# Kernel tuning notes

Measured on AMD Instinct MI355X. Metric: run time of the kernel, lower is better.

## Reference

```python
import jax, jax.numpy as jnp
import numpy as np

E, B, T = 7, 50, 100               # ensemble (network_size), no_batches=50, time blocks
D, A, L, H, C = 128, 32, 256, 1024, 128  # data, action, latent, hidden, context sizes
H_STEP = 0.1                        # (t1 - t0) / T == dt -> one SDE step per block


def setup_inputs() -> dict:
    key = jax.random.key(0)
    ks = iter(jax.random.split(key, 64))
    def nrm(shape, scale=1.0):
        return jax.random.normal(next(ks), shape, jnp.float32) * scale
    def ens(i, o):
        s = 1.0 / np.sqrt(i)
        return nrm((E, i, o), s), nrm((E, o), s)
    def lin(i, o):
        s = 1.0 / np.sqrt(i)
        return nrm((i, o), s), nrm((o,), s)
    inp = {}
    inp["enc_w1"], inp["enc_b1"] = ens(D, H)
    inp["enc_w2"], inp["enc_b2"] = ens(H, H)
    inp["enc_w3"], inp["enc_b3"] = ens(H, C)
    inp["qz0_w"], inp["qz0_b"] = ens(C, 2 * L)
    inp["act_w"], inp["act_b"] = ens(L + A + D, L)
    inp["proj_w1"], inp["proj_b1"] = ens(L, H)
    inp["proj_w2"], inp["proj_b2"] = ens(H, H)
    inp["proj_w3"], inp["proj_b3"] = ens(H, D)
    inp["f_w1"], inp["f_b1"] = lin(L, H)
    inp["f_w2"], inp["f_b2"] = lin(H, H)
    inp["f_w3"], inp["f_b3"] = lin(H, L)
    inp["h_w1"], inp["h_b1"] = lin(L, H)
    inp["h_w2"], inp["h_b2"] = lin(H, H)
    inp["h_w3"], inp["h_b3"] = lin(H, L)
    # per-latent-dim g nets: Linear(1,H) -> ReLU -> Linear(H,1), stacked over L dims
    inp["g_w1"] = nrm((L, H), 0.2)
    inp["g_b1"] = nrm((L, H), 0.2)
    inp["g_w2"] = nrm((L, H), 0.2 / np.sqrt(H))
    inp["g_b2"] = 0.5 + nrm((L,), 0.01)   # keep diffusion bounded away from 0
    inp["pz0_mean"] = jnp.zeros((E, 1, L), jnp.float32)
    inp["pz0_logstd"] = jnp.zeros((E, 1, L), jnp.float32)
    inp["xs"] = nrm((E, T * B, D))
    inp["actions"] = nrm((E, T * B, A))
    inp["eps_z0"] = nrm((T, E, B, L))      # torch.randn_like noise for z0 reparam
    inp["dw_noise"] = nrm((T, E * B, L))   # Brownian increment noise (unit std)
    return inp


def reference(enc_w1, enc_b1, enc_w2, enc_b2, enc_w3, enc_b3,
              qz0_w, qz0_b, act_w, act_b,
              proj_w1, proj_b1, proj_w2, proj_b2, proj_w3, proj_b3,
              f_w1, f_b1, f_w2, f_b2, f_w3, f_b3,
              h_w1, h_b1, h_w2, h_b2, h_w3, h_b3,
              g_w1, g_b1, g_w2, g_b2,
              pz0_mean, pz0_logstd,
              xs, actions, eps_z0, dw_noise):
    def ens_lin(x, w, b):  # EnsembleFC: bmm + bias
        return jnp.einsum('ebi,eio->ebo', x, w) + b[:, None, :]

    def encoder(x):
        x = jax.nn.relu(ens_lin(x, enc_w1, enc_b1))
        x = jax.nn.relu(ens_lin(x, enc_w2, enc_b2))
        return ens_lin(x, enc_w3, enc_b3)

    def projector(z):
        z = jnp.tanh(ens_lin(z, proj_w1, proj_b1))
        z = jnp.tanh(ens_lin(z, proj_w2, proj_b2))
        return ens_lin(z, proj_w3, proj_b3)

    def mlp(y, w1, b1, w2, b2, w3, b3):  # Linear-ReLU-Linear-Tanh-Linear
        y = jax.nn.relu(y @ w1 + b1)
        y = jnp.tanh(y @ w2 + b2)
        return y @ w3 + b3

    def g_fn(y):  # vectorized per-dim tiny MLPs: y (N, L) -> (N, L)
        hh = jax.nn.relu(y[:, :, None] * g_w1[None] + g_b1[None])  # (N, L, H)
        return jnp.sum(hh * g_w2[None], axis=-1) + g_b2

    xs_t = jnp.moveaxis(xs.reshape(E, T, B, D), 1, 0)        # (T, E, B, D)
    act_t = jnp.moveaxis(actions.reshape(E, T, B, A), 1, 0)  # (T, E, B, A)
    sqrt_h = jnp.sqrt(jnp.float32(H_STEP))

    def step(carry, inps):
        zs_last, i = carry
        x_i, a_i, eps_i, dw_i = inps
        ctx = encoder(x_i)                                  # (E, B, C)
        q = ens_lin(ctx, qz0_w, qz0_b)                      # (E, B, 2L)
        qm, ql = q[..., :L], q[..., L:]
        z0 = qm + jnp.exp(ql) * eps_i
        z_in = jnp.where(i == 0, z0, zs_last)               # first step uses z0
        lad = jnp.concatenate([z_in, a_i, x_i], axis=2)
        z = ens_lin(lad, act_w, act_b).reshape(E * B, L)
        # one SDE step with logqp (f: posterior drift, h: prior drift, g: diffusion)
        fv = mlp(z, f_w1, f_b1, f_w2, f_b2, f_w3, f_b3)
        hv = mlp(z, h_w1, h_b1, h_w2, h_b2, h_w3, h_b3)
        gv = g_fn(z)
        u = (fv - hv) / gv
        lr = 0.5 * jnp.sum(u * u, axis=-1) * H_STEP         # (E*B,) log-ratio increment
        z_new = z + fv * H_STEP + gv * (sqrt_h * dw_i)
        zs_new = z_new.reshape(E, B, L)
        xm = projector(zs_new)                              # (E, B, D)
        # KL(q(z0) || p(z0)) for diagonal Gaussians
        kl = (pz0_logstd - ql) \
             + (jnp.exp(2.0 * ql) + (qm - pz0_mean) ** 2) / (2.0 * jnp.exp(2.0 * pz0_logstd)) \
             - 0.5
        logqp0 = kl.sum(axis=2).mean(axis=1)                # (E,)
        lr_mean = lr.reshape(E, B).mean(axis=1)             # (E,)
        return (zs_new, i + 1), (lr_mean, logqp0, xm)

    init = (jnp.zeros((E, B, L), xs.dtype), jnp.int32(0))
    (_, _), (lrm, lq0, xms) = jax.lax.scan(step, init, (xs_t, act_t, eps_z0, dw_noise))
    logqp_path = lrm.sum(axis=0) + lq0.sum(axis=0)          # (E,)
    predicted_xs = jnp.moveaxis(xms, 0, 1).reshape(E, T * B, D)
    return logqp_path, predicted_xs
```

## Files before the change

kernel.cpp:

```cpp
#include <hip/hip_runtime.h>
#include <hip/hip_bf16.h>
#include <math.h>

#define E_ 7
#define B_ 50
#define T_ 100
#define D_ 128
#define A_ 32
#define L_ 256
#define H_ 1024
#define C_ 128
#define EB_ 350
#define TB_ 5000
#define SQRTH 0.31622776601683794f

typedef __attribute__((ext_vector_type(8))) short s8v;
typedef __attribute__((ext_vector_type(4))) float f32x4;
typedef _Float16 f16x2 __attribute__((ext_vector_type(2)));
typedef __hip_bfloat16 bf16;

#define MFMA __builtin_amdgcn_mfma_f32_16x16x32_bf16

__device__ __forceinline__ int lswz(int row, int ck) {
  return ((ck & ~7) | ((ck ^ row) & 7)) << 3;
}

struct BG {
  const bf16* A[8];
  const bf16* W[8];
  const float* bias[8];
  float* Cf[8];
  bf16* Cb[8];
};

template<int BM, int ACT, int OUT>
__global__ __launch_bounds__(256)
void bgemm(BG g, int M, int K, int lda, int ldw, int ldc) {
  __shared__ short As[BM * 64];
  __shared__ short Ws[128 * 64];
  const short* Ap = (const short*)g.A[blockIdx.z];
  const short* Wp = (const short*)g.W[blockIdx.z];
  const int bm = blockIdx.x * BM, bn = blockIdx.y * 128;
  const int tid = threadIdx.x;
  const int wv = tid >> 6, lane = tid & 63;
  const int wm0 = (wv >> 1) * (BM / 2), wn0 = (wv & 1) * 64;
  const int l15 = lane & 15, l4 = lane >> 4;
  constexpr int FM = BM / 32;
  constexpr int AI = BM / 32;
  f32x4 acc[FM][4] = {};
  for (int k0 = 0; k0 < K; k0 += 64) {
    s8v av[AI], wvv[4];
#pragma unroll
    for (int i = 0; i < AI; ++i) {
      const int c = tid + i * 256, r = c >> 3, ck = c & 7;
      s8v v = {};
      if (bm + r < M) v = *(const s8v*)(Ap + (size_t)(bm + r) * lda + k0 + ck * 8);
      av[i] = v;
// ... 108 lines not shown
  const bf16 h = __float2bfloat16(w);
  const size_t fo = (size_t)e * 65536 + ((size_t)(n >> 4) * 8 + (k >> 5)) * 512 +
                    (((k >> 3) & 3) << 7) + ((n & 15) << 3) + (k & 7);
  hi[fo] = h;
  lo[fo] = __float2bfloat16(w - __bfloat162float(h));
}

__global__ __launch_bounds__(256)
void ax_build(const float* __restrict__ actions, const float* __restrict__ xs,
              bf16* __restrict__ dst) {
  const int idx = blockIdx.x * 256 + threadIdx.x;
  if (idx >= E_ * TB_ * 192) return;
  const int k = idx % 192;
  const int r = (idx / 192) % TB_;
  const int e = idx / (192 * TB_);
  float v = 0.f;
  if (k < 32) v = actions[((size_t)e * TB_ + r) * A_ + k];
  else if (k < 160) v = xs[((size_t)e * TB_ + r) * D_ + (k - 32)];
  dst[idx] = __float2bfloat16(v);
}

__global__ __launch_bounds__(256)
void waxT_build(const float* __restrict__ act_w, bf16* __restrict__ dst) {
  const int idx = blockIdx.x * 256 + threadIdx.x;
  if (idx >= E_ * 256 * 192) return;
  const int k = idx % 192;
  const int n = (idx / 192) % 256;
  const int e = idx / (192 * 256);
  float v = (k < 160) ? act_w[(size_t)e * 416 * 256 + (size_t)(256 + k) * 256 + n] : 0.f;
  dst[idx] = __float2bfloat16(v);
}

__global__ __launch_bounds__(256)
void gpack_build(const float* __restrict__ gw1, const float* __restrict__ gb1,
                 const float* __restrict__ gw2, _Float16* __restrict__ dst) {
  const int idx = blockIdx.x * 256 + threadIdx.x;
  if (idx >= 256 * 3 * 1024) return;
  const int l = idx / 3072, rem = idx - l * 3072, arr = rem >> 10, h = rem & 1023;
  const float* s = arr == 0 ? gw1 : (arr == 1 ? gb1 : gw2);
  dst[idx] = (_Float16)s[(size_t)l * 1024 + h];
}

__global__ __launch_bounds__(256)
void qkl_kernel(const float* __restrict__ ctx, int rows, int row_off, int ctx_estride,
                const float* __restrict__ qw, const float* __restrict__ qb,
                const float* __restrict__ pm, const float* __restrict__ pl,
                const float* __restrict__ eps0, bf16* __restrict__ z0hi,
                bf16* __restrict__ z0lo, float* __restrict__ logqp) {
  __shared__ float cx[16][128];
  __shared__ float red[16];
  const int e = blockIdx.y;
  const int r0 = blockIdx.x * 16;
  const int tid = threadIdx.x;
  {
    const int r = tid >> 4, c = (tid & 15) * 8;
    float4 v0 = make_float4(0.f, 0.f, 0.f, 0.f), v1 = v0;
    if (r0 + r < rows) {
      const float* src = ctx + (size_t)e * ctx_estride + (size_t)(r0 + r) * C_ + c;
      v0 = *(const float4*)src;
      v1 = *(const float4*)(src + 4);
    }
    *(float4*)&cx[r][c] = v0;
    *(float4*)&cx[r][c + 4] = v1;
  }
  if (tid < 16) red[tid] = 0.f;
  __syncthreads();
  const int j = tid;
  const float* w = qw + (size_t)e * C_ * 512;
  float am_[16] = {};
  float al_[16] = {};
  for (int k0 = 0; k0 < C_; k0 += 4) {
    float wm[4], wl[4];
#pragma unroll
// ... 11 lines not shown
        al_[r] = fmaf(cc[q], wl[q], al_[r]);
      }
    }
  }
  const float qbm = qb[(size_t)e * 512 + j];
  const float qbl = qb[(size_t)e * 512 + 256 + j];
  const float pmv = pm[(size_t)e * L_ + j];
  const float plv = pl[(size_t)e * L_ + j];
  const float inv2e = 0.5f * expf(-2.f * plv);
#pragma unroll
  for (int r = 0; r < 16; ++r) {
    float kl = 0.f;
    if (r0 + r < rows) {
      const float qm_ = am_[r] + qbm;
      const float ql_ = al_[r] + qbl;
      const float dm = qm_ - pmv;
      kl = plv - ql_ + (expf(2.f * ql_) + dm * dm) * inv2e - 0.5f;
      const int gi = row_off + r0 + r;
      if (gi < B_) {
        const size_t zi = ((size_t)e * B_ + gi) * L_ + j;
        const float z0 = qm_ + expf(ql_) * eps0[zi];
        const bf16 h = __float2bfloat16(z0);
        z0hi[zi] = h;
        z0lo[zi] = __float2bfloat16(z0 - __bfloat162float(h));
      }
    }
    for (int off = 32; off; off >>= 1) kl += __shfl_xor(kl, off, 64);
    if ((tid & 63) == 0) atomicAdd(&red[r], kl);
  }
  __syncthreads();
  if (tid < 16 && r0 + tid < rows) atomicAdd(&logqp[e], red[tid] * (1.0f / B_));
}

__global__ __launch_bounds__(256, 2)
void k1_act(const bf16* __restrict__ zhi, const bf16* __restrict__ zlo,
            const bf16* __restrict__ wzh, const bf16* __restrict__ wzl,
            const float* __restrict__ axw, float* __restrict__ zP,
            bf16* __restrict__ zPb, int t) {
  __shared__ short Ah[16 * 256];
  __shared__ short Al[16 * 256];
  const int e = blockIdx.z, rb = blockIdx.x, nb = blockIdx.y * 128;
  const int r0 = rb * 13;
  const int nrows = (50 - r0 < 13) ? (50 - r0) : 13;
  const int tid = threadIdx.x, lane = tid & 63, wv = tid >> 6;
  const int l15 = lane & 15, l4 = lane >> 4;
  const short* zh = (const short*)zhi + (size_t)(e * 50 + r0) * 256;
  const short* zl = (const short*)zlo + (size_t)(e * 50 + r0) * 256;
#pragma unroll
  for (int i = 0; i < 2; ++i) {
    const int lin = tid + i * 256, row = lin >> 5, ck = lin & 31;
    s8v vh = {}, vl = {};
    if (row < nrows) {
      vh = *(const s8v*)(zh + row * 256 + ck * 8);
      vl = *(const s8v*)(zl + row * 256 + ck * 8);
    }
    *(s8v*)(Ah + row * 256 + lswz(row, ck)) = vh;
    *(s8v*)(Al + row * 256 + lswz(row, ck)) = vl;
  }
  __syncthreads();
  const short* Bh = (const short*)wzh + (size_t)e * 65536;
  const short* Bl = (const short*)wzl + (size_t)e * 65536;
  f32x4 acc[2] = {};
#pragma unroll
  for (int kt = 0; kt < 8; ++kt) {
    const int ck = kt * 4 + l4;
    const s8v ah = *(const s8v*)(Ah + l15 * 256 + lswz(l15, ck));
    const s8v al = *(const s8v*)(Al + l15 * 256 + lswz(l15, ck));
#pragma unroll
    for (int nt = 0; nt < 2; ++nt) {
      const int ng = nb + wv * 32 + nt * 16;
      const size_t bo = ((size_t)(ng >> 4) * 8 + kt) * 512 + lane * 8;
      const s8v bh = *(const s8v*)(Bh + bo);
      const s8v bl = *(const s8v*)(Bl + bo);
      acc[nt] = MFMA(ah, bh, acc[nt], 0, 0, 0);
      acc[nt] = MFMA(al, bh, acc[nt], 0, 0, 0);
      acc[nt] = MFMA(ah, bl, acc[nt], 0, 0, 0);
    }
  }
#pragma unroll
  for (int nt = 0; nt < 2; ++nt) {
    const int col = nb + wv * 32 + nt * 16 + l15;
#pragma unroll
    for (int j = 0; j < 4; ++j) {
      const int row = l4 * 4 + j;
      if (row < nrows) {
        const int gr = e * 50 + r0 + row;
        const float v = acc[nt][j] + axw[((size_t)e * TB_ + t * 50 + r0 + row) * 256 + col];
        zP[(size_t)gr * 256 + col] = v;
        zPb[(size_t)gr * 256 + col] = __float2bfloat16(v);
      }
    }
  }
}

__global__ __launch_bounds__(256, 2)
void k2_l1(const bf16* __restrict__ zPb, const bf16* __restrict__ w1f,
           const float* __restrict__ fb1, const float* __restrict__ hb1,
           bf16* __restrict__ fh1) {
  __shared__ short As[16 * 256];
  const int rb = blockIdx.x, nb = blockIdx.y * 128;
  const int r0 = rb * 16;
  const int tid = threadIdx.x, lane = tid & 63, wv = tid >> 6;
  const int l15 = lane & 15, l4 = lane >> 4;
#pragma unroll
  for (int i = 0; i < 2; ++i) {
    const int lin = tid + i * 256, row = lin >> 5, ck = lin & 31;
    s8v v = {};
    if (r0 + row < EB_)
      v = *(const s8v*)((const short*)zPb + (size_t)(r0 + row) * 256 + ck * 8);
    *(s8v*)(As + row * 256 + lswz(row, ck)) = v;
  }
  __syncthreads();
  f32x4 acc[2] = {};
#pragma unroll
  for (int kt = 0; kt < 8; ++kt) {
    const int ck = kt * 4 + l4;
    const s8v a = *(const s8v*)(As + l15 * 256 + lswz(l15, ck));
#pragma unroll
    for (int nt = 0; nt < 2; ++nt) {
      const int ng = nb + wv * 32 + nt * 16;
      const s8v b = *(const s8v*)((const short*)w1f + ((size_t)(ng >> 4) * 8 + kt) * 512 + lane * 8);
      acc[nt] = MFMA(a, b, acc[nt], 0, 0, 0);
    }
  }
#pragma unroll
  for (int nt = 0; nt < 2; ++nt) {
    const int col = nb + wv * 32 + nt * 16 + l15;
    const float bv = (col < 1024) ? fb1[col] : hb1[col - 1024];
#pragma unroll
    for (int j = 0; j < 4; ++j) {
      const int row = r0 + l4 * 4 + j;
      if (row < EB_)
        fh1[(size_t)row * 2048 + col] = __float2bfloat16(fmaxf(acc[nt][j] + bv, 0.f));
    }
  }
}

__global__ __launch_bounds__(256, 2)
void k3_l2(const bf16* __restrict__ fh1, const bf16* __restrict__ w2f,
           const float* __restrict__ fb2, const float* __restrict__ hb2,
           bf16* __restrict__ fh2) {
  __shared__ short As[16 * 1024];
  const int rb = blockIdx.x, nbl = blockIdx.y;
  const int nb = nbl * 128, r0 = rb * 16;
  const int half = (nbl >= 8) ? 1024 : 0;
  const int tid = threadIdx.x, lane = tid & 63, wv = tid >> 6;
  const int l15 = lane & 15, l4 = lane >> 4;
#pragma unroll
  for (int i = 0; i < 8; ++i) {
    const int lin = tid + i * 256, row = lin >> 7, ck = lin & 127;
    s8v v = {};
    if (r0 + row < EB_)
      v = *(const s8v*)((const short*)fh1 + (size_t)(r0 + row) * 2048 + half + ck * 8);
    *(s8v*)(As + row * 1024 + lswz(row, ck)) = v;
  }
  __syncthreads();
  f32x4 acc[2] = {};
#pragma unroll 4
  for (int kt = 0; kt < 32; ++kt) {
    const int ck = kt * 4 + l4;
    const s8v a = *(const s8v*)(As + l15 * 1024 + lswz(l15, ck));
#pragma unroll
    for (int nt = 0; nt < 2; ++nt) {
      const int ng = nb + wv * 32 + nt * 16;
      const s8v b = *(const s8v*)((const short*)w2f + ((size_t)(ng >> 4) * 32 + kt) * 512 + lane * 8);
      acc[nt] = MFMA(a, b, acc[nt], 0, 0, 0);
    }
  }
#pragma unroll
  for (int nt = 0; nt < 2; ++nt) {
    const int col = nb + wv * 32 + nt * 16 + l15;
    const float bv = half ? hb2[col - 1024] : fb2[col];
#pragma unroll
    for (int j = 0; j < 4; ++j) {
      const int row = r0 + l4 * 4 + j;
      if (row < EB_)
        fh2[(size_t)row * 2048 + col] = __float2bfloat16(tanhf(acc[nt][j] + bv));
    }
  }
}

__global__ __launch_bounds__(256, 1)
void k4_fin(const bf16* __restrict__ fh2, const bf16* __restrict__ w3f,
            const float* __restrict__ fb3, const float* __restrict__ hb3,
            const _Float16* __restrict__ gpk, const float* __restrict__ gb2,
            const float* __restrict__ zP, const float* __restrict__ dw,
            bf16* __restrict__ zhi, bf16* __restrict__ zlo,
            bf16* __restrict__ zs_bf, float* __restrict__ logqp, int t) {
  __shared__ short As[16 * 1024];
  __shared__ float ztile[16][64];
  __shared__ float gvt[16][64];
  __shared__ float ebuck[8];
  const int rb = blockIdx.x, cb = blockIdx.y;
  const int r0 = rb * 16, c0 = cb * 64;
  const int tid = threadIdx.x, lane = tid & 63, wv = tid >> 6;
  const int l15 = lane & 15, l4 = lane >> 4;
  if (tid < 8) ebuck[tid] = 0.f;
#pragma unroll
  for (int i = 0; i < 4; ++i) {
    const int lin = tid + i * 256, row = lin >> 6, col = lin & 63;
    ztile[row][col] = (r0 + row < EB_) ? zP[(size_t)(r0 + row) * 256 + c0 + col] : 1.0f;
  }
  f32x4 accF = {}, accH = {};
#pragma unroll
  for (int fb = 0; fb < 2; ++fb) {
    __syncthreads();
#pragma unroll
    for (int i = 0; i < 8; ++i) {
      const int lin = tid + i * 256, row = lin >> 7, ck = lin & 127;
      s8v v = {};
      if (r0 + row < EB_)
        v = *(const s8v*)((const short*)fh2 + (size_t)(r0 + row) * 2048 + fb * 1024 + ck * 8);
      *(s8v*)(As + row * 1024 + lswz(row, ck)) = v;
    }
    __syncthreads();
    const int ng = fb * 256 + c0 + wv * 16;
    f32x4 acc = {};
#pragma unroll 4
    for (int kt = 0; kt < 32; ++kt) {
      const int ck = kt * 4 + l4;
      const s8v a = *(const s8v*)(As + l15 * 1024 + lswz(l15, ck));
      const s8v b = *(const s8v*)((const short*)w3f + ((size_t)(ng >> 4) * 32 + kt) * 512 + lane * 8);
      acc = MFMA(a, b, acc, 0, 0, 0);
    }
    if (fb) accH = acc; else accF = acc;
  }
  __syncthreads();
  {
    const int lloc = tid >> 2, hq = tid & 3;
    const _Float16* gl = gpk + (size_t)(c0 + lloc) * 3072 + hq * 256;
    f16x2 z2[16];
#pragma unroll
    for (int r = 0; r < 16; ++r) {
      const _Float16 zh_ = (_Float16)ztile[r][lloc];
      z2[r] = f16x2{zh_, zh_};
    }
    float ga[16] = {};
    for (int hp = 0; hp < 128; ++hp) {
      const f16x2 w1v = *(const f16x2*)(gl + 2 * hp);
      const f16x2 b1v = *(const f16x2*)(gl + 1024 + 2 * hp);
      const f16x2 w2v = *(const f16x2*)(gl + 2048 + 2 * hp);
#pragma unroll
      for (int r = 0; r < 16; ++r) {
        f16x2 tt = z2[r] * w1v + b1v;
#if __has_builtin(__builtin_elementwise_max)
        const f16x2 zz = {};
        tt = __builtin_elementwise_max(tt, zz);
#else
        tt[0] = tt[0] > (_Float16)0 ? tt[0] : (_Float16)0;
        tt[1] = tt[1] > (_Float16)0 ? tt[1] : (_Float16)0;
#endif
#if __has_builtin(__builtin_amdgcn_fdot2)
        ga[r] = __builtin_amdgcn_fdot2(tt, w2v, ga[r], false);
#else
        ga[r] += (float)tt[0] * (float)w2v[0] + (float)tt[1] * (float)w2v[1];
#endif
      }
    }
#pragma unroll
    for (int r = 0; r < 16; ++r) {
      float v = ga[r];
      v += __shfl_xor(v, 1, 64);
      v += __shfl_xor(v, 2, 64);
      if (hq == 0) gvt[r][lloc] = v + gb2[c0 + lloc];
    }
  }
  __syncthreads();
  const int col_loc = wv * 16 + l15, col = c0 + col_loc;
  const float fb3v = fb3[col], hb3v = hb3[col];
#pragma unroll
  for (int j = 0; j < 4; ++j) {
    const int rl = l4 * 4 + j, row = r0 + rl;
    if (row < EB_) {
      const float fv = accF[j] + fb3v;
      const float hv = accH[j] + hb3v;
      const float gv = gvt[rl][col_loc];
      const float u = (fv - hv) / gv;
      atomicAdd(&ebuck[row / 50], 0.001f * u * u);
      const float znew = ztile[rl][col_loc] + 0.1f * fv +
                         gv * (SQRTH * dw[(size_t)t * (EB_ * 256) + (size_t)row * 256 + col]);
      const bf16 h = __float2bfloat16(znew);
      const size_t zi = (size_t)row * 256 + col;
      zhi[zi] = h;
      zlo[zi] = __float2bfloat16(znew - __bfloat162float(h));
      const int e = row / 50, b = row - e * 50;
      zs_bf[((size_t)e * TB_ + t * 50 + b) * 256 + col] = h;
    }
  }
  __syncthreads();
  if (tid < 7) {
    const float v = ebuck[tid];
    if (v != 0.f) atomicAdd(&logqp[tid], v);
  }
}

__global__ void init_kernel(float* logqp) {
  if (threadIdx.x < E_) logqp[threadIdx.x] = 0.f;
}

extern "C" void kernel_launch(void* const* d_in, const int* in_sizes, int n_in,
                              void* d_out, int out_size, void* d_ws, size_t ws_size,
                              hipStream_t stream) {
  (void)in_sizes; (void)n_in; (void)out_size;
  const float* enc_w1 = (const float*)d_in[0];
  const float* enc_b1 = (const float*)d_in[1];
  const float* enc_w2 = (const float*)d_in[2];
  const float* enc_b2 = (const float*)d_in[3];
  const float* enc_w3 = (const float*)d_in[4];
  const float* enc_b3 = (const float*)d_in[5];
  const float* qz0_w  = (const float*)d_in[6];
  const float* qz0_b  = (const float*)d_in[7];
  const float* act_w  = (const float*)d_in[8];
  const float* act_b  = (const float*)d_in[9];
  const float* proj_w1 = (const float*)d_in[10];
  const float* proj_b1 = (const float*)d_in[11];
  const float* proj_w2 = (const float*)d_in[12];
  const float* proj_b2 = (const float*)d_in[13];
  const float* proj_w3 = (const float*)d_in[14];
  const float* proj_b3 = (const float*)d_in[15];
  const float* f_w1 = (const float*)d_in[16];
  const float* f_b1 = (const float*)d_in[17];
  const float* f_w2 = (const float*)d_in[18];
  const float* f_b2 = (const float*)d_in[19];
  const float* f_w3 = (const float*)d_in[20];
  const float* f_b3 = (const float*)d_in[21];
  const float* h_w1 = (const float*)d_in[22];
  const float* h_b1 = (const float*)d_in[23];
  const float* h_w2 = (const float*)d_in[24];
  const float* h_b2 = (const float*)d_in[25];
  const float* h_w3 = (const float*)d_in[26];
  const float* h_b3 = (const float*)d_in[27];
  const float* g_w1 = (const float*)d_in[28];
  const float* g_b1 = (const float*)d_in[29];
  const float* g_w2 = (const float*)d_in[30];
  const float* g_b2 = (const float*)d_in[31];
  const float* pz0_mean   = (const float*)d_in[32];
  const float* pz0_logstd = (const float*)d_in[33];
  const float* xs      = (const float*)d_in[34];
  const float* actions = (const float*)d_in[35];
  const float* eps_z0  = (const float*)d_in[36];
  const float* dw      = (const float*)d_in[37];

  float* out = (float*)d_out;
  float* logqp = out;
  float* pred = out + E_;

  char* base = (char*)d_ws;
  size_t off = 0;
  auto alloc = [&](size_t bytes) {
    void* p = base + off;
    off = (off + bytes + 255) & ~(size_t)255;
    return p;
  };
  bf16* zhi    = (bf16*)alloc((size_t)EB_ * 256 * 2);
  bf16* zlo    = (bf16*)alloc((size_t)EB_ * 256 * 2);
  float* zP    = (float*)alloc((size_t)EB_ * 256 * 4);
  bf16* zPb    = (bf16*)alloc((size_t)EB_ * 256 * 2);
  bf16* fh1    = (bf16*)alloc((size_t)EB_ * 2048 * 2);
  bf16* fh2    = (bf16*)alloc((size_t)EB_ * 2048 * 2);
  bf16* zs_bf  = (bf16*)alloc((size_t)E_ * T_ * B_ * 256 * 2);
  float* axw   = (float*)alloc((size_t)E_ * TB_ * 256 * 4);
  bf16* ax_bf  = (bf16*)alloc((size_t)E_ * TB_ * 192 * 2);
  bf16* waxT   = (bf16*)alloc((size_t)E_ * 256 * 192 * 2);
  bf16* wzh    = (bf16*)alloc((size_t)E_ * 65536 * 2);
  bf16* wzl    = (bf16*)alloc((size_t)E_ * 65536 * 2);
  bf16* w1f    = (bf16*)alloc((size_t)2048 * 256 * 2);
  bf16* w2f    = (bf16*)alloc((size_t)2048 * 1024 * 2);
  bf16* w3f    = (bf16*)alloc((size_t)512 * 1024 * 2);
  _Float16* gpk = (_Float16*)alloc((size_t)256 * 3 * 1024 * 2);
  bf16* xs_bf  = (bf16*)alloc((size_t)E_ * TB_ * D_ * 2);
  bf16* ew1T = (bf16*)alloc((size_t)E_ * D_ * H_ * 2);
  bf16* ew2T = (bf16*)alloc((size_t)E_ * H_ * H_ * 2);
  bf16* ew3T = (bf16*)alloc((size_t)E_ * H_ * C_ * 2);
  bf16* pw1T = (bf16*)alloc((size_t)E_ * L_ * H_ * 2);
  bf16* pw2T = (bf16*)alloc((size_t)E_ * H_ * H_ * 2);
  bf16* pw3T = (bf16*)alloc((size_t)E_ * H_ * D_ * 2);
  const size_t per_row = (size_t)E_ * (H_ * 2 * 2 + C_ * 4);
  size_t remain = (ws_size > off + 4096) ? (ws_size - off - 4096) : 0;
  int CH = (int)(remain / per_row);
  if (CH > 2500) CH = 2500;
  if (CH < 64) CH = 64;
  bf16* bufA = (bf16*)alloc((size_t)E_ * CH * H_ * 2);
  bf16* bufB = (bf16*)alloc((size_t)E_ * CH * H_ * 2);
  float* bufC = (float*)alloc((size_t)E_ * CH * C_ * 4);

  init_kernel<<<dim3(1), dim3(64), 0, stream>>>(logqp);

  const dim3 cb256(256);
  cvt_kernel<<<dim3((E_ * TB_ * D_ / 4 + 255) / 256), cb256, 0, stream>>>(xs, xs_bf, E_ * TB_ * D_ / 4);
  cvtT_kernel<<<dim3(H_ / 32, D_ / 32, E_), cb256, 0, stream>>>(enc_w1, ew1T, D_, H_, (long)D_ * H_, (long)D_ * H_);
  cvtT_kernel<<<dim3(H_ / 32, H_ / 32, E_), cb256, 0, stream>>>(enc_w2, ew2T, H_, H_, (long)H_ * H_, (long)H_ * H_);
  cvtT_kernel<<<dim3(C_ / 32, H_ / 32, E_), cb256, 0, stream>>>(enc_w3, ew3T, H_, C_, (long)H_ * C_, (long)H_ * C_);
  cvtT_kernel<<<dim3(H_ / 32, L_ / 32, E_), cb256, 0, stream>>>(proj_w1, pw1T, L_, H_, (long)L_ * H_, (long)L_ * H_);
  cvtT_kernel<<<dim3(H_ / 32, H_ / 32, E_), cb256, 0, stream>>>(proj_w2, pw2T, H_, H_, (long)H_ * H_, (long)H_ * H_);
  cvtT_kernel<<<dim3(D_ / 32, H_ / 32, E_), cb256, 0, stream>>>(proj_w3, pw3T, H_, D_, (long)H_ * D_, (long)H_ * D_);
  ax_build<<<dim3((E_ * TB_ * 192 + 255) / 256), cb256, 0, stream>>>(actions, xs, ax_bf);
  waxT_build<<<dim3((E_ * 256 * 192 + 255) / 256), cb256, 0, stream>>>(act_w, waxT);
  packWz<<<dim3((E_ * 65536 + 255) / 256), cb256, 0, stream>>>(act_w, wzh, wzl);
  packW<<<dim3((256 * 1024 + 255) / 256), cb256, 0, stream>>>(f_w1, w1f, 256, 1024);
  packW<<<dim3((256 * 1024 + 255) / 256), cb256, 0, stream>>>(h_w1, w1f + (size_t)1024 * 256, 256, 1024);
  packW<<<dim3((1024 * 1024 + 255) / 256), cb256, 0, stream>>>(f_w2, w2f, 1024, 1024);
  packW<<<dim3((1024 * 1024 + 255) / 256), cb256, 0, stream>>>(h_w2, w2f + (size_t)1024 * 1024, 1024, 1024);
  packW<<<dim3((1024 * 256 + 255) / 256), cb256, 0, stream>>>(f_w3, w3f, 1024, 256);
  packW<<<dim3((1024 * 256 + 255) / 256), cb256, 0, stream>>>(h_w3, w3f + (size_t)256 * 1024, 1024, 256);
  gpack_build<<<dim3((256 * 3 * 1024 + 255) / 256), cb256, 0, stream>>>(g_w1, g_b1, g_w2, gpk);

  BG g;
  for (int e = 0; e < E_; ++e) {
    g.A[e] = ax_bf + (size_t)e * TB_ * 192;
    g.W[e] = waxT + (size_t)e * 256 * 192;
    g.bias[e] = act_b + (size_t)e * 256;
    g.Cf[e] = axw + (size_t)e * TB_ * 256;
  }
  bgemm<128, 0, 0><<<dim3((TB_ + 127) / 128, 2, E_), 256, 0, stream>>>(g, TB_, 192, 192, 192, 256);

  for (int c = 0; c < TB_; c += CH) {
    const int rows = (TB_ - c < CH) ? (TB_ - c) : CH;
    const int mt = (rows + 127) / 128;
    for (int e = 0; e < E_; ++e) {
      g.A[e] = xs_bf + ((size_t)e * TB_ + c) * D_;
      g.W[e] = ew1T + (size_t)e * D_ * H_;
      g.bias[e] = enc_b1 + (size_t)e * H_;
      g.Cb[e] = bufA + (size_t)e * CH * H_;
    }
    bgemm<128, 1, 1><<<dim3(mt, H_ / 128, E_), 256, 0, stream>>>(g, rows, D_, D_, D_, H_);
    for (int e = 0; e < E_; ++e) {
      g.A[e] = bufA + (size_t)e * CH * H_;
      g.W[e] = ew2T + (size_t)e * H_ * H_;
      g.bias[e] = enc_b2 + (size_t)e * H_;
      g.Cb[e] = bufB + (size_t)e * CH * H_;
    }
    bgemm<128, 1, 1><<<dim3(mt, H_ / 128, E_), 256, 0, stream>>>(g, rows, H_, H_, H_, H_);
    for (int e = 0; e < E_; ++e) {
      g.A[e] = bufB + (size_t)e * CH * H_;
      g.W[e] = ew3T + (size_t)e * H_ * C_;
      g.bias[e] = enc_b3 + (size_t)e * C_;
      g.Cf[e] = bufC + (size_t)e * CH * C_;
    }
    bgemm<128, 0, 0><<<dim3(mt, C_ / 128, E_), 256, 0, stream>>>(g, rows, H_, H_, H_, C_);
    qkl_kernel<<<dim3((rows + 15) / 16, E_), 256, 0, stream>>>(
        bufC, rows, c, CH * C_, qz0_w, qz0_b, pz0_mean, pz0_logstd, eps_z0,
        zhi, zlo, logqp);
  }

  for (int t = 0; t < T_; ++t) {
    k1_act<<<dim3(4, 2, E_), 256, 0, stream>>>(zhi, zlo, wzh, wzl, axw, zP, zPb, t);
    k2_l1<<<dim3(22, 16), 256, 0, stream>>>(zPb, w1f, f_b1, h_b1, fh1);
    k3_l2<<<dim3(22, 16), 256, 0, stream>>>(fh1, w2f, f_b2, h_b2, fh2);
    k4_fin<<<dim3(22, 4), 256, 0, stream>>>(fh2, w3f, f_b3, h_b3, gpk, g_b2,
                                            zP, dw, zhi, zlo, zs_bf, logqp, t);
  }

  for (int c = 0; c < TB_; c += CH) {
    const int rows = (TB_ - c < CH) ? (TB_ - c) : CH;
    const int mt = (rows + 127) / 128;
    for (int e = 0; e < E_; ++e) {
      g.A[e] = zs_bf + ((size_t)e * T_ * B_ + c) * L_;
      g.W[e] = pw1T + (size_t)e * L_ * H_;
      g.bias[e] = proj_b1 + (size_t)e * H_;
      g.Cb[e] = bufA + (size_t)e * CH * H_;
    }
    bgemm<128, 2, 1><<<dim3(mt, H_ / 128, E_), 256, 0, stream>>>(g, rows, L_, L_, L_, H_);
    for (int e = 0; e < E_; ++e) {
      g.A[e] = bufA + (size_t)e * CH * H_;
      g.W[e] = pw2T + (size_t)e * H_ * H_;
      g.bias[e] = proj_b2 + (size_t)e * H_;
      g.Cb[e] = bufB + (size_t)e * CH * H_;
    }
    bgemm<128, 2, 1><<<dim3(mt, H_ / 128, E_), 256, 0, stream>>>(g, rows, H_, H_, H_, H_);
    for (int e = 0; e < E_; ++e) {
      g.A[e] = bufB + (size_t)e * CH * H_;
      g.W[e] = pw3T + (size_t)e * H_ * D_;
      g.bias[e] = proj_b3 + (size_t)e * D_;
      g.Cf[e] = pred + ((size_t)e * TB_ + c) * D_;
    }
    bgemm<128, 0, 0><<<dim3(mt, D_ / 128, E_), 256, 0, stream>>>(g, rows, H_, H_, H_, D_);
  }
}
```

Baseline: 10.30 ms.

## Fuse action-latent GEMM with first f/h MLP layer into one kernel

Merges k1_act and k2_l1 into a single kernel per ensemble member and column tile. Each block recomputes the full 50x256 action-latent projection into shared memory as bf16, then runs the first f/h layer from it, which removes one launch per time step and the zPb round trip through global memory. In exchange the projection GEMM is computed redundantly in all 16 column blocks, and the launch uses fewer, larger blocks (112) with 96KB of shared memory each, which lowers occupancy.

```diff
diff --git a/kernel.cpp b/kernel.cpp
--- a/kernel.cpp
+++ b/kernel.cpp
@@ -22,7 +22,11 @@
 #define MFMA __builtin_amdgcn_mfma_f32_16x16x32_bf16
 
 __device__ __forceinline__ int lswz(int row, int ck) {
-  return ((ck & ~7) | ((ck ^ row) & 7)) << 3;
+  return (((ck & ~7) | ((ck ^ row) & 7)) << 3);
+}
+__device__ __forceinline__ int swzE(int r, int col) {
+  const int ck = col >> 3;
+  return (((ck & ~7) | ((ck ^ r) & 7)) << 3) + (col & 7);
 }
 
 struct BG {
@@ -281,106 +285,87 @@
   if (tid < 16 && r0 + tid < rows) atomicAdd(&logqp[e], red[tid] * (1.0f / B_));
 }
 
-__global__ __launch_bounds__(256, 2)
-void k1_act(const bf16* __restrict__ zhi, const bf16* __restrict__ zlo,
+__global__ __launch_bounds__(256)
+void akt_l1(const bf16* __restrict__ zhi, const bf16* __restrict__ zlo,
             const bf16* __restrict__ wzh, const bf16* __restrict__ wzl,
-            const float* __restrict__ axw, float* __restrict__ zP,
-            bf16* __restrict__ zPb, int t) {
-  __shared__ short Ah[16 * 256];
-  __shared__ short Al[16 * 256];
-  const int e = blockIdx.z, rb = blockIdx.x, nb = blockIdx.y * 128;
-  const int r0 = rb * 13;
-  const int nrows = (50 - r0 < 13) ? (50 - r0) : 13;
+            const float* __restrict__ axw, const bf16* __restrict__ w1f,
+            const float* __restrict__ fb1, const float* __restrict__ hb1,
+            float* __restrict__ zP, bf16* __restrict__ fh1, int t) {
+  __shared__ short Zh[64 * 256];
+  __shared__ short Zl[64 * 256];
+  __shared__ short Pb[64 * 256];
+  const int e = blockIdx.y, nt1 = blockIdx.x;
   const int tid = threadIdx.x, lane = tid & 63, wv = tid >> 6;
   const int l15 = lane & 15, l4 = lane >> 4;
-  const short* zh = (const short*)zhi + (size_t)(e * 50 + r0) * 256;
-  const short* zl = (const short*)zlo + (size_t)(e * 50 + r0) * 256;
-#pragma unroll
-  for (int i = 0; i < 2; ++i) {
-    const int lin = tid + i * 256, row = lin >> 5, ck = lin & 31;
+  for (int i = tid; i < 64 * 32; i += 256) {
+    const int row = i >> 5, ck = i & 31;
     s8v vh = {}, vl = {};
-    if (row < nrows) {
-      vh = *(const s8v*)(zh + row * 256 + ck * 8);
-      vl = *(const s8v*)(zl + row * 256 + ck * 8);
-    }
-    *(s8v*)(Ah + row * 256 + lswz(row, ck)) = vh;
-    *(s8v*)(Al + row * 256 + lswz(row, ck)) = vl;
+    if (row < 50) {
+      vh = *(const s8v*)((const short*)zhi + (size_t)(e * 50 + row) * 256 + ck * 8);
+      vl = *(const s8v*)((const short*)zlo + (size_t)(e * 50 + row) * 256 + ck * 8);
+    }
+    *(s8v*)(Zh + row * 256 + lswz(row, ck)) = vh;
+    *(s8v*)(Zl + row * 256 + lswz(row, ck)) = vl;
   }
   __syncthreads();
   const short* Bh = (const short*)wzh + (size_t)e * 65536;
   const short* Bl = (const short*)wzl + (size_t)e * 65536;
-  f32x4 acc[2] = {};
-#pragma unroll
-  for (int kt = 0; kt < 8; ++kt) {
-    const int ck = kt * 4 + l4;
-    const s8v ah = *(const s8v*)(Ah + l15 * 256 + lswz(l15, ck));
-    const s8v al = *(const s8v*)(Al + l15 * 256 + lswz(l15, ck));
-#pragma unroll
-    for (int nt = 0; nt < 2; ++nt) {
-      const int ng = nb + wv * 32 + nt * 16;
-      const size_t bo = ((size_t)(ng >> 4) * 8 + kt) * 512 + lane * 8;
-      const s8v bh = *(const s8v*)(Bh + bo);
-      const s8v bl = *(const s8v*)(Bl + bo);
-      acc[nt] = MFMA(ah, bh, acc[nt], 0, 0, 0);
-      acc[nt] = MFMA(al, bh, acc[nt], 0, 0, 0);
-      acc[nt] = MFMA(ah, bl, acc[nt], 0, 0, 0);
-    }
-  }
-#pragma unroll
-  for (int nt = 0; nt < 2; ++nt) {
-    const int col = nb + wv * 32 + nt * 16 + l15;
-#pragma unroll
-    for (int j = 0; j < 4; ++j) {
-      const int row = l4 * 4 + j;
-      if (row < nrows) {
-        const int gr = e * 50 + r0 + row;
-        const float v = acc[nt][j] + axw[((size_t)e * TB_ + t * 50 + r0 + row) * 256 + col];
-        zP[(size_t)gr * 256 + col] = v;
-        zPb[(size_t)gr * 256 + col] = __float2bfloat16(v);
-      }
-    }
-  }
-}
-
-__global__ __launch_bounds__(256, 2)
-void k2_l1(const bf16* __restrict__ zPb, const bf16* __restrict__ w1f,
-           const float* __restrict__ fb1, const float* __restrict__ hb1,
-           bf16* __restrict__ fh1) {
-  __shared__ short As[16 * 256];
-  const int rb = blockIdx.x, nb = blockIdx.y * 128;
-  const int r0 = rb * 16;
-  const int tid = threadIdx.x, lane = tid & 63, wv = tid >> 6;
-  const int l15 = lane & 15, l4 = lane >> 4;
-#pragma unroll
-  for (int i = 0; i < 2; ++i) {
-    const int lin = tid + i * 256, row = lin >> 5, ck = lin & 31;
-    s8v v = {};
-    if (r0 + row < EB_)
-      v = *(const s8v*)((const short*)zPb + (size_t)(r0 + row) * 256 + ck * 8);
-    *(s8v*)(As + row * 256 + lswz(row, ck)) = v;
-  }
-  __syncthreads();
-  f32x4 acc[2] = {};
-#pragma unroll
-  for (int kt = 0; kt < 8; ++kt) {
-    const int ck = kt * 4 + l4;
-    const s8v a = *(const s8v*)(As + l15 * 256 + lswz(l15, ck));
-#pragma unroll
-    for (int nt = 0; nt < 2; ++nt) {
-      const int ng = nb + wv * 32 + nt * 16;
-      const s8v b = *(const s8v*)((const short*)w1f + ((size_t)(ng >> 4) * 8 + kt) * 512 + lane * 8);
-      acc[nt] = MFMA(a, b, acc[nt], 0, 0, 0);
-    }
-  }
-#pragma unroll
-  for (int nt = 0; nt < 2; ++nt) {
-    const int col = nb + wv * 32 + nt * 16 + l15;
-    const float bv = (col < 1024) ? fb1[col] : hb1[col - 1024];
-#pragma unroll
-    for (int j = 0; j < 4; ++j) {
-      const int row = r0 + l4 * 4 + j;
-      if (row < EB_)
-        fh1[(size_t)row * 2048 + col] = __float2bfloat16(fmaxf(acc[nt][j] + bv, 0.f));
+#pragma unroll
+  for (int c2 = 0; c2 < 4; ++c2) {
+    const int ct = wv * 4 + c2;
+#pragma unroll
+    for (int rt = 0; rt < 4; ++rt) {
+      f32x4 acc = {};
+#pragma unroll
+      for (int kt = 0; kt < 8; ++kt) {
+        const int ck = kt * 4 + l4;
+        const int ar = rt * 16 + l15;
+        const s8v ah = *(const s8v*)(Zh + ar * 256 + lswz(ar, ck));
+        const s8v al = *(const s8v*)(Zl + ar * 256 + lswz(ar, ck));
+        const size_t bo = ((size_t)(ct * 8 + kt)) * 512 + (size_t)lane * 8;
+        const s8v bh = *(const s8v*)(Bh + bo);
+        const s8v bl = *(const s8v*)(Bl + bo);
+        acc = MFMA(ah, bh, acc, 0, 0, 0);
+        acc = MFMA(al, bh, acc, 0, 0, 0);
+        acc = MFMA(ah, bl, acc, 0, 0, 0);
+      }
+      const int col = ct * 16 + l15;
+#pragma unroll
+      for (int j = 0; j < 4; ++j) {
+        const int r = rt * 16 + l4 * 4 + j;
+        float v = 0.f;
+        if (r < 50)
+          v = acc[j] + axw[((size_t)(e * TB_) + t * 50 + r) * 256 + col];
+        *(bf16*)&Pb[r * 256 + swzE(r, col)] = __float2bfloat16(v);
+        if (nt1 == 0 && r < 50) zP[(size_t)(e * 50 + r) * 256 + col] = v;
+      }
+    }
+  }
+  __syncthreads();
+#pragma unroll
+  for (int c2 = 0; c2 < 2; ++c2) {
+    const int gct = nt1 * 8 + wv * 2 + c2;
+#pragma unroll
+    for (int rt = 0; rt < 4; ++rt) {
+      f32x4 acc = {};
+#pragma unroll
+      for (int kt = 0; kt < 8; ++kt) {
+        const int ck = kt * 4 + l4;
+        const int ar = rt * 16 + l15;
+        const s8v av = *(const s8v*)(Pb + ar * 256 + lswz(ar, ck));
+        const s8v bv = *(const s8v*)((const short*)w1f +
+                                     ((size_t)(gct * 8 + kt)) * 512 + (size_t)lane * 8);
+        acc = MFMA(av, bv, acc, 0, 0, 0);
+      }
+      const int col = gct * 16 + l15;
+      const float bv_ = (col < 1024) ? fb1[col] : hb1[col - 1024];
+#pragma unroll
+      for (int j = 0; j < 4; ++j) {
+        const int r = rt * 16 + l4 * 4 + j;
+        if (r < 50)
+          fh1[(size_t)(e * 50 + r) * 2048 + col] =
+              __float2bfloat16(fmaxf(acc[j] + bv_, 0.f));
+      }
     }
   }
 }
@@ -604,7 +589,6 @@
   bf16* zhi    = (bf16*)alloc((size_t)EB_ * 256 * 2);
   bf16* zlo    = (bf16*)alloc((size_t)EB_ * 256 * 2);
   float* zP    = (float*)alloc((size_t)EB_ * 256 * 4);
-  bf16* zPb    = (bf16*)alloc((size_t)EB_ * 256 * 2);
   bf16* fh1    = (bf16*)alloc((size_t)EB_ * 2048 * 2);
   bf16* fh2    = (bf16*)alloc((size_t)EB_ * 2048 * 2);
   bf16* zs_bf  = (bf16*)alloc((size_t)E_ * T_ * B_ * 256 * 2);
@@ -693,8 +677,8 @@
   }
 
   for (int t = 0; t < T_; ++t) {
-    k1_act<<<dim3(4, 2, E_), 256, 0, stream>>>(zhi, zlo, wzh, wzl, axw, zP, zPb, t);
-    k2_l1<<<dim3(22, 16), 256, 0, stream>>>(zPb, w1f, f_b1, h_b1, fh1);
+    akt_l1<<<dim3(16, E_), 256, 0, stream>>>(zhi, zlo, wzh, wzl, axw, w1f,
+                                             f_b1, h_b1, zP, fh1, t);
     k3_l2<<<dim3(22, 16), 256, 0, stream>>>(fh1, w2f, f_b2, h_b2, fh2);
     k4_fin<<<dim3(22, 4), 256, 0, stream>>>(fh2, w3f, f_b3, h_b3, gpk, g_b2,
                                             zP, dw, zhi, zlo, zs_bf, logqp, t);
```

New measurement: 11.53 ms. 1.12x slower.

## Fuse SDE finalize with next step's action and layer-1 GEMMs per ensemble

Applied to the files above, without the earlier changes.

Replaces the per-step k4_fin/k1_act/k2_l1 sequence with one kernel, kfin, plus k3_l2, so each time step launches two kernels instead of four. Each kfin block owns a quarter of one ensemble's batch rows across all 256 latent columns. It computes the layer-3 drift outputs, the g diffusion net, the state update, the next action projection, and the next layer-1 activations while keeping z in shared memory. The g-weight packing is reordered for coalesced half2 loads, and the log-ratio sum is reduced per block. In exchange the fused kernel runs only 28 blocks of 512 threads, which lowers parallelism and could make each step slower despite fewer launches and less global traffic.

```diff
diff --git a/kernel.cpp b/kernel.cpp
--- a/kernel.cpp
+++ b/kernel.cpp
@@ -22,7 +22,28 @@
 #define MFMA __builtin_amdgcn_mfma_f32_16x16x32_bf16
 
 __device__ __forceinline__ int lswz(int row, int ck) {
-  return ((ck & ~7) | ((ck ^ row) & 7)) << 3;
+  return (((ck & ~7) | ((ck ^ row) & 7)) << 3);
+}
+__device__ __forceinline__ int swzE(int r, int col) {
+  const int ck = col >> 3;
+  return (((ck & ~7) | ((ck ^ r) & 7)) << 3) + (col & 7);
+}
+__device__ __forceinline__ f16x2 relu2(f16x2 t) {
+#if __has_builtin(__builtin_elementwise_max)
+  const f16x2 zz = {};
+  return __builtin_elementwise_max(t, zz);
+#else
+  t[0] = t[0] > (_Float16)0 ? t[0] : (_Float16)0;
+  t[1] = t[1] > (_Float16)0 ? t[1] : (_Float16)0;
+  return t;
+#endif
+}
+__device__ __forceinline__ float fdot2a(f16x2 a, f16x2 b, float c) {
+#if __has_builtin(__builtin_amdgcn_fdot2)
+  return __builtin_amdgcn_fdot2(a, b, c, false);
+#else
+  return c + (float)a[0] * (float)b[0] + (float)a[1] * (float)b[1];
+#endif
 }
 
 struct BG {
@@ -197,13 +218,16 @@
 }
 
 __global__ __launch_bounds__(256)
-void gpack_build(const float* __restrict__ gw1, const float* __restrict__ gb1,
-                 const float* __restrict__ gw2, _Float16* __restrict__ dst) {
+void gpack2(const float* __restrict__ gw1, const float* __restrict__ gb1,
+            const float* __restrict__ gw2, _Float16* __restrict__ dst) {
   const int idx = blockIdx.x * 256 + threadIdx.x;
-  if (idx >= 256 * 3 * 1024) return;
-  const int l = idx / 3072, rem = idx - l * 3072, arr = rem >> 10, h = rem & 1023;
+  if (idx >= 3 * 512 * 256 * 2) return;
+  const int i = idx & 1;
+  const int l = (idx >> 1) & 255;
+  const int hpg = (idx >> 9) & 511;
+  const int arr = idx >> 18;
   const float* s = arr == 0 ? gw1 : (arr == 1 ? gb1 : gw2);
-  dst[idx] = (_Float16)s[(size_t)l * 1024 + h];
+  dst[idx] = (_Float16)s[(size_t)l * 1024 + hpg * 2 + i];
 }
 
 __global__ __launch_bounds__(256)
@@ -429,117 +453,197 @@
   }
 }
 
-__global__ __launch_bounds__(256, 1)
-void k4_fin(const bf16* __restrict__ fh2, const bf16* __restrict__ w3f,
-            const float* __restrict__ fb3, const float* __restrict__ hb3,
-            const _Float16* __restrict__ gpk, const float* __restrict__ gb2,
-            const float* __restrict__ zP, const float* __restrict__ dw,
-            bf16* __restrict__ zhi, bf16* __restrict__ zlo,
-            bf16* __restrict__ zs_bf, float* __restrict__ logqp, int t) {
+__global__ __launch_bounds__(512)
+void kfin(const bf16* __restrict__ fh2, const bf16* __restrict__ w3f,
+          const float* __restrict__ fb3, const float* __restrict__ hb3,
+          const _Float16* __restrict__ gpk, const float* __restrict__ gb2,
+          float* __restrict__ zP, const float* __restrict__ dw,
+          const float* __restrict__ axw, const bf16* __restrict__ wzh,
+          const bf16* __restrict__ wzl, const bf16* __restrict__ w1f,
+          const float* __restrict__ fb1, const float* __restrict__ hb1,
+          bf16* __restrict__ zs_bf, bf16* __restrict__ fh1,
+          float* __restrict__ logqp, int t, int doAct) {
   __shared__ short As[16 * 1024];
-  __shared__ float ztile[16][64];
-  __shared__ float gvt[16][64];
-  __shared__ float ebuck[8];
-  const int rb = blockIdx.x, cb = blockIdx.y;
-  const int r0 = rb * 16, c0 = cb * 64;
-  const int tid = threadIdx.x, lane = tid & 63, wv = tid >> 6;
+  __shared__ float zst[16 * 256];
+  __shared__ float gvt[16 * 256];
+  __shared__ short Zh[16 * 256];
+  __shared__ short Zl[16 * 256];
+  __shared__ short Pb[16 * 256];
+  __shared__ float red[8];
+  const int bx = blockIdx.x;
+  const int e = bx >> 2, q = bx & 3;
+  const int nr = (q < 2) ? 13 : 12;
+  const int b0 = (q < 2) ? q * 13 : 26 + (q - 2) * 12;
+  const int R0 = e * 50 + b0;
+  const int tid = threadIdx.x, wave = tid >> 6, lane = tid & 63;
   const int l15 = lane & 15, l4 = lane >> 4;
-  if (tid < 8) ebuck[tid] = 0.f;
-#pragma unroll
-  for (int i = 0; i < 4; ++i) {
-    const int lin = tid + i * 256, row = lin >> 6, col = lin & 63;
-    ztile[row][col] = (r0 + row < EB_) ? zP[(size_t)(r0 + row) * 256 + c0 + col] : 1.0f;
-  }
-  f32x4 accF = {}, accH = {};
-#pragma unroll
-  for (int fb = 0; fb < 2; ++fb) {
+  for (int i = tid; i < 4096; i += 512) {
+    const int r = i >> 8, c = i & 255;
+    zst[i] = (r < nr) ? zP[(size_t)(R0 + r) * 256 + c] : 0.f;
+  }
+  for (int i = tid; i < 2048; i += 512) {
+    const int row = i >> 7, ck = i & 127;
+    s8v v = {};
+    if (row < nr) v = *(const s8v*)((const short*)fh2 + (size_t)(R0 + row) * 2048 + ck * 8);
+    *(s8v*)(As + row * 1024 + lswz(row, ck)) = v;
+  }
+  __syncthreads();
+  f32x4 accF[2] = {}, accH[2] = {};
+#pragma unroll 4
+  for (int kt = 0; kt < 32; ++kt) {
+    const int ck = kt * 4 + l4;
+    const s8v a = *(const s8v*)(As + l15 * 1024 + lswz(l15, ck));
+#pragma unroll
+    for (int cc = 0; cc < 2; ++cc) {
+      const int ct = wave * 2 + cc;
+      const s8v b = *(const s8v*)((const short*)w3f + ((size_t)(ct * 32 + kt)) * 512 + (size_t)lane * 8);
+      accF[cc] = MFMA(a, b, accF[cc], 0, 0, 0);
+    }
+  }
+  __syncthreads();
+  for (int i = tid; i < 2048; i += 512) {
+    const int row = i >> 7, ck = i & 127;
+    s8v v = {};
+    if (row < nr) v = *(const s8v*)((const short*)fh2 + (size_t)(R0 + row) * 2048 + 1024 + ck * 8);
+    *(s8v*)(As + row * 1024 + lswz(row, ck)) = v;
+  }
+  __syncthreads();
+#pragma unroll 4
+  for (int kt = 0; kt < 32; ++kt) {
+    const int ck = kt * 4 + l4;
+    const s8v a = *(const s8v*)(As + l15 * 1024 + lswz(l15, ck));
+#pragma unroll
+    for (int cc = 0; cc < 2; ++cc) {
+      const int ct = 16 + wave * 2 + cc;
+      const s8v b = *(const s8v*)((const short*)w3f + ((size_t)(ct * 32 + kt)) * 512 + (size_t)lane * 8);
+      accH[cc] = MFMA(a, b, accH[cc], 0, 0, 0);
+    }
+  }
+  {
+    const int hh = wave >> 2;
+    const int l = tid & 255;
+    f16x2 z2[13];
+    float ga[13];
+#pragma unroll
+    for (int r = 0; r < 13; ++r) {
+      const _Float16 z = (_Float16)zst[r * 256 + l];
+      z2[r] = f16x2{z, z};
+      ga[r] = 0.f;
+    }
+    const _Float16* gb_ = gpk + (size_t)(hh * 256) * 512 + (size_t)l * 2;
+    for (int k = 0; k < 256; ++k) {
+      const size_t o = (size_t)k * 512;
+      const f16x2 w1 = *(const f16x2*)(gb_ + o);
+      const f16x2 b1 = *(const f16x2*)(gb_ + 262144 + o);
+      const f16x2 w2 = *(const f16x2*)(gb_ + 524288 + o);
+#pragma unroll
+      for (int r = 0; r < 13; ++r)
+        ga[r] = fdot2a(relu2(z2[r] * w1 + b1), w2, ga[r]);
+    }
+    if (hh == 0) {
+#pragma unroll
+      for (int r = 0; r < 13; ++r) gvt[r * 256 + l] = ga[r];
+    }
     __syncthreads();
-#pragma unroll
-    for (int i = 0; i < 8; ++i) {
-      const int lin = tid + i * 256, row = lin >> 7, ck = lin & 127;
-      s8v v = {};
-      if (r0 + row < EB_)
-        v = *(const s8v*)((const short*)fh2 + (size_t)(r0 + row) * 2048 + fb * 1024 + ck * 8);
-      *(s8v*)(As + row * 1024 + lswz(row, ck)) = v;
-    }
-    __syncthreads();
-    const int ng = fb * 256 + c0 + wv * 16;
+    if (hh == 1) {
+#pragma unroll
+      for (int r = 0; r < 13; ++r) gvt[r * 256 + l] += ga[r] + gb2[l];
+    }
+  }
+  __syncthreads();
+  float lr = 0.f;
+#pragma unroll
+  for (int cc = 0; cc < 2; ++cc) {
+    const int col = (wave * 2 + cc) * 16 + l15;
+    const float fb3v = fb3[col], hb3v = hb3[col];
+#pragma unroll
+    for (int j = 0; j < 4; ++j) {
+      const int r = l4 * 4 + j;
+      if (r < nr) {
+        const float fv = accF[cc][j] + fb3v;
+        const float hv = accH[cc][j] + hb3v;
+        const float gv = gvt[r * 256 + col];
+        const float u = (fv - hv) / gv;
+        lr += u * u;
+        const float zn = zst[r * 256 + col] + 0.1f * fv +
+            gv * (SQRTH * dw[(size_t)t * (EB_ * 256) + (size_t)(R0 + r) * 256 + col]);
+        zst[r * 256 + col] = zn;
+        zs_bf[((size_t)e * TB_ + t * 50 + b0 + r) * 256 + col] = __float2bfloat16(zn);
+      }
+    }
+  }
+#pragma unroll
+  for (int o = 32; o; o >>= 1) lr += __shfl_xor(lr, o, 64);
+  if (lane == 0) red[wave] = lr;
+  __syncthreads();
+  if (tid == 0) {
+    float s = 0.f;
+    for (int w = 0; w < 8; ++w) s += red[w];
+    atomicAdd(&logqp[e], 0.001f * s);
+  }
+  if (!doAct) return;
+  __syncthreads();
+  {
+    const int row = tid >> 5, ck = tid & 31;
+    const int base = row * 256;
+    const int so = base + lswz(row, ck);
+#pragma unroll
+    for (int m = 0; m < 8; ++m) {
+      const float f = zst[base + ck * 8 + m];
+      const bf16 h = __float2bfloat16(f);
+      const bf16 lo = __float2bfloat16(f - __bfloat162float(h));
+      *(bf16*)&Zh[so + m] = h;
+      *(bf16*)&Zl[so + m] = lo;
+    }
+  }
+  __syncthreads();
+#pragma unroll
+  for (int cc = 0; cc < 2; ++cc) {
+    const int ct = wave * 2 + cc;
     f32x4 acc = {};
-#pragma unroll 4
-    for (int kt = 0; kt < 32; ++kt) {
+#pragma unroll
+    for (int kt = 0; kt < 8; ++kt) {
       const int ck = kt * 4 + l4;
-      const s8v a = *(const s8v*)(As + l15 * 1024 + lswz(l15, ck));
-      const s8v b = *(const s8v*)((const short*)w3f + ((size_t)(ng >> 4) * 32 + kt) * 512 + lane * 8);
+      const s8v ah = *(const s8v*)(Zh + l15 * 256 + lswz(l15, ck));
+      const s8v al = *(const s8v*)(Zl + l15 * 256 + lswz(l15, ck));
+      const size_t bo = ((size_t)(ct * 8 + kt)) * 512 + (size_t)lane * 8;
+      const s8v bh = *(const s8v*)((const short*)wzh + (size_t)e * 65536 + bo);
+      const s8v bl = *(const s8v*)((const short*)wzl + (size_t)e * 65536 + bo);
+      acc = MFMA(ah, bh, acc, 0, 0, 0);
+      acc = MFMA(al, bh, acc, 0, 0, 0);
+      acc = MFMA(ah, bl, acc, 0, 0, 0);
+    }
+    const int col = ct * 16 + l15;
+#pragma unroll
+    for (int j = 0; j < 4; ++j) {
+      const int r = l4 * 4 + j;
+      float v = 0.f;
+      if (r < nr) {
+        v = acc[j] + axw[((size_t)e * TB_ + (t + 1) * 50 + b0 + r) * 256 + col];
+        zP[(size_t)(R0 + r) * 256 + col] = v;
+      }
+      *(bf16*)&Pb[r * 256 + swzE(r, col)] = __float2bfloat16(v);
+    }
+  }
+  __syncthreads();
+  for (int c = 0; c < 16; ++c) {
+    const int gct = wave * 16 + c;
+    f32x4 acc = {};
+#pragma unroll
+    for (int kt = 0; kt < 8; ++kt) {
+      const int ck = kt * 4 + l4;
+      const s8v a = *(const s8v*)(Pb + l15 * 256 + lswz(l15, ck));
+      const s8v b = *(const s8v*)((const short*)w1f + ((size_t)(gct * 8 + kt)) * 512 + (size_t)lane * 8);
       acc = MFMA(a, b, acc, 0, 0, 0);
     }
-    if (fb) accH = acc; else accF = acc;
-  }
-  __syncthreads();
-  {
-    const int lloc = tid >> 2, hq = tid & 3;
-    const _Float16* gl = gpk + (size_t)(c0 + lloc) * 3072 + hq * 256;
-    f16x2 z2[16];
-#pragma unroll
-    for (int r = 0; r < 16; ++r) {
-      const _Float16 zh_ = (_Float16)ztile[r][lloc];
-      z2[r] = f16x2{zh_, zh_};
-    }
-    float ga[16] = {};
-    for (int hp = 0; hp < 128; ++hp) {
-      const f16x2 w1v = *(const f16x2*)(gl + 2 * hp);
-      const f16x2 b1v = *(const f16x2*)(gl + 1024 + 2 * hp);
-      const f16x2 w2v = *(const f16x2*)(gl + 2048 + 2 * hp);
-#pragma unroll
-      for (int r = 0; r < 16; ++r) {
-        f16x2 tt = z2[r] * w1v + b1v;
-#if __has_builtin(__builtin_elementwise_max)
-        const f16x2 zz = {};
-        tt = __builtin_elementwise_max(tt, zz);
-#else
-        tt[0] = tt[0] > (_Float16)0 ? tt[0] : (_Float16)0;
-        tt[1] = tt[1] > (_Float16)0 ? tt[1] : (_Float16)0;
-#endif
-#if __has_builtin(__builtin_amdgcn_fdot2)
-        ga[r] = __builtin_amdgcn_fdot2(tt, w2v, ga[r], false);
-#else
-        ga[r] += (float)tt[0] * (float)w2v[0] + (float)tt[1] * (float)w2v[1];
-#endif
-      }
-    }
-#pragma unroll
-    for (int r = 0; r < 16; ++r) {
-      float v = ga[r];
-      v += __shfl_xor(v, 1, 64);
-      v += __shfl_xor(v, 2, 64);
-      if (hq == 0) gvt[r][lloc] = v + gb2[c0 + lloc];
-    }
-  }
-  __syncthreads();
-  const int col_loc = wv * 16 + l15, col = c0 + col_loc;
-  const float fb3v = fb3[col], hb3v = hb3[col];
-#pragma unroll
-  for (int j = 0; j < 4; ++j) {
-    const int rl = l4 * 4 + j, row = r0 + rl;
-    if (row < EB_) {
-      const float fv = accF[j] + fb3v;
-      const float hv = accH[j] + hb3v;
-      const float gv = gvt[rl][col_loc];
-      const float u = (fv - hv) / gv;
-      atomicAdd(&ebuck[row / 50], 0.001f * u * u);
-      const float znew = ztile[rl][col_loc] + 0.1f * fv +
-                         gv * (SQRTH * dw[(size_t)t * (EB_ * 256) + (size_t)row * 256 + col]);
-      const bf16 h = __float2bfloat16(znew);
-      const size_t zi = (size_t)row * 256 + col;
-      zhi[zi] = h;
-      zlo[zi] = __float2bfloat16(znew - __bfloat162float(h));
-      const int e = row / 50, b = row - e * 50;
-      zs_bf[((size_t)e * TB_ + t * 50 + b) * 256 + col] = h;
-    }
-  }
-  __syncthreads();
-  if (tid < 7) {
-    const float v = ebuck[tid];
-    if (v != 0.f) atomicAdd(&logqp[tid], v);
+    const int col = gct * 16 + l15;
+    const float bv = (col < 1024) ? fb1[col] : hb1[col - 1024];
+#pragma unroll
+    for (int j = 0; j < 4; ++j) {
+      const int r = l4 * 4 + j;
+      if (r < nr)
+        fh1[(size_t)(R0 + r) * 2048 + col] = __float2bfloat16(fmaxf(acc[j] + bv, 0.f));
+    }
   }
 }
 
@@ -608,7 +712,7 @@
   bf16* fh1    = (bf16*)alloc((size_t)EB_ * 2048 * 2);
   bf16* fh2    = (bf16*)alloc((size_t)EB_ * 2048 * 2);
   bf16* zs_bf  = (bf16*)alloc((size_t)E_ * T_ * B_ * 256 * 2);
-  float* axw   = (float*)alloc((size_t)E_ * TB_ * 256 * 4);
+  float* axw   = (float*)alloc((size_t)E_ * TB_ * 256 * 4 + 256 * 64);
   bf16* ax_bf  = (bf16*)alloc((size_t)E_ * TB_ * 192 * 2);
   bf16* waxT   = (bf16*)alloc((size_t)E_ * 256 * 192 * 2);
   bf16* wzh    = (bf16*)alloc((size_t)E_ * 65536 * 2);
@@ -616,7 +720,7 @@
   bf16* w1f    = (bf16*)alloc((size_t)2048 * 256 * 2);
   bf16* w2f    = (bf16*)alloc((size_t)2048 * 1024 * 2);
   bf16* w3f    = (bf16*)alloc((size_t)512 * 1024 * 2);
-  _Float16* gpk = (_Float16*)alloc((size_t)256 * 3 * 1024 * 2);
+  _Float16* gpk = (_Float16*)alloc((size_t)3 * 512 * 256 * 2 * 2);
   bf16* xs_bf  = (bf16*)alloc((size_t)E_ * TB_ * D_ * 2);
   bf16* ew1T = (bf16*)alloc((size_t)E_ * D_ * H_ * 2);
   bf16* ew2T = (bf16*)alloc((size_t)E_ * H_ * H_ * 2);
@@ -652,7 +756,7 @@
   packW<<<dim3((1024 * 1024 + 255) / 256), cb256, 0, stream>>>(h_w2, w2f + (size_t)1024 * 1024, 1024, 1024);
   packW<<<dim3((1024 * 256 + 255) / 256), cb256, 0, stream>>>(f_w3, w3f, 1024, 256);
   packW<<<dim3((1024 * 256 + 255) / 256), cb256, 0, stream>>>(h_w3, w3f + (size_t)256 * 1024, 1024, 256);
-  gpack_build<<<dim3((256 * 3 * 1024 + 255) / 256), cb256, 0, stream>>>(g_w1, g_b1, g_w2, gpk);
+  gpack2<<<dim3((3 * 512 * 256 * 2 + 255) / 256), cb256, 0, stream>>>(g_w1, g_b1, g_w2, gpk);
 
   BG g;
   for (int e = 0; e < E_; ++e) {
@@ -692,12 +796,14 @@
         zhi, zlo, logqp);
   }
 
+  k1_act<<<dim3(4, 2, E_), 256, 0, stream>>>(zhi, zlo, wzh, wzl, axw, zP, zPb, 0);
+  k2_l1<<<dim3(22, 16), 256, 0, stream>>>(zPb, w1f, f_b1, h_b1, fh1);
   for (int t = 0; t < T_; ++t) {
-    k1_act<<<dim3(4, 2, E_), 256, 0, stream>>>(zhi, zlo, wzh, wzl, axw, zP, zPb, t);
-    k2_l1<<<dim3(22, 16), 256, 0, stream>>>(zPb, w1f, f_b1, h_b1, fh1);
     k3_l2<<<dim3(22, 16), 256, 0, stream>>>(fh1, w2f, f_b2, h_b2, fh2);
-    k4_fin<<<dim3(22, 4), 256, 0, stream>>>(fh2, w3f, f_b3, h_b3, gpk, g_b2,
-                                            zP, dw, zhi, zlo, zs_bf, logqp, t);
+    kfin<<<dim3(28), dim3(512), 0, stream>>>(fh2, w3f, f_b3, h_b3, gpk, g_b2,
+                                             zP, dw, axw, wzh, wzl, w1f,
+                                             f_b1, h_b1, zs_bf, fh1, logqp,
+                                             t, (t + 1 < T_) ? 1 : 0);
   }
 
   for (int c = 0; c < TB_; c += CH) {
```

After: 12.90 ms. +25.3%, slower.
